# Kernel optimization log

Hardware: AMD Instinct MI355X
Metric: run time of the kernel (lower is better)

## Reference

```python
import jax, jax.numpy as jnp
import numpy as np

RADIUS = 5
WIN = (RADIUS - 1) * 2 + 1  # 9


def setup_inputs() -> dict:
    key = jax.random.key(0)
    k1, k2 = jax.random.split(key)
    B, K, H, W = 4, 4, 224, 224
    seg = jax.random.uniform(k1, (B, K, H, W), dtype=jnp.float32)
    weight = jax.random.uniform(k2, (B, 1, H, W, WIN, WIN), dtype=jnp.float32)
    return {"seg": seg, "weight": weight}


def reference(seg, weight):
    # seg: [B,K,H,W]; weight: [B,1,H,W,w,w] local affinity window, w = 2*(radius-1)+1
    B, K, H, W = seg.shape
    Kconst = jnp.float32(K)
    # torch pads by `radius` on all sides but only uses window offsets 0..2*(radius-1),
    # i.e. relative offsets [-radius, radius-2] -- replicate exactly.
    padded = jnp.pad(seg, ((0, 0), (0, 0), (RADIUS, RADIUS), (RADIUS, RADIUS)))
    # weighted sum over the local window without materializing [B,K,H,W,w,w]
    sum_w_seg = jnp.zeros_like(seg)
    for m in range(WIN):
        for n in range(WIN):
            sum_w_seg = sum_w_seg + padded[:, :, m:m + H, n:n + W] * weight[:, :, :, :, m, n]
    assocA = jnp.sum(sum_w_seg * seg, axis=(-1, -2))                      # [B,K]
    assocV = jnp.sum(jnp.sum(weight, axis=(-1, -2)) * seg, axis=(-1, -2))  # [B,K]
    assoc = jnp.sum(assocA / assocV, axis=-1)                              # [B]
    return jnp.sum(Kconst - assoc)
```

## Files before the change

### kernel.cpp

```cpp
#include <hip/hip_runtime.h>

#define RADIUS 5
#define WIN 9
#define BB 4
#define KK 4
#define HH 224
#define WW 224
#define HW (HH * WW)
#define PD 234
#define PAREA (PD * PD)
#define NBUCKET 64
#define PARTIAL_FLOATS (NBUCKET * BB * 8)
#define WAVES_PER_B (HW / 64)
#define ELEMS_PER_WAVE (64 * 81)


__global__ __launch_bounds__(256) void ncuts_pad(
    const float* __restrict__ seg, float4* __restrict__ pseg)
{
    const int tid = blockIdx.x * 256 + threadIdx.x;
    if (tid >= BB * PAREA) return;
    const int b  = tid / PAREA;
    const int rc = tid - b * PAREA;
    const int r  = rc / PD;
    const int c  = rc - r * PD;
    const int hh = r - RADIUS;
    const int ww = c - RADIUS;
    float4 v = {0.f, 0.f, 0.f, 0.f};
    if (hh >= 0 && hh < HH && ww >= 0 && ww < WW) {
        const float* sb = seg + (size_t)b * KK * HW + hh * WW + ww;
        v.x = sb[0 * HW];
        v.y = sb[1 * HW];
        v.z = sb[2 * HW];
        v.w = sb[3 * HW];
    }
    pseg[tid] = v;
}

__global__ __launch_bounds__(256, 4) void ncuts_main(
    const float* __restrict__ weight,
    const float4* __restrict__ pseg,
    float* __restrict__ partial)
{
    const int lane = threadIdx.x & 63;
    const int wid  = blockIdx.x * 4 + (threadIdx.x >> 6);
    const int b    = wid / WAVES_PER_B;

    const float* wbase = weight + (size_t)wid * ELEMS_PER_WAVE;
    const float4* p4   = pseg + (size_t)b * PAREA;

    const int pix0 = wid * 64;
    const int rem0 = pix0 - b * HW;
    int h = rem0 / WW;
    int w = rem0 - h * WW;
    int rowoff = h * PD + w;
    int tap = lane;

    float a0 = 0.f, a1 = 0.f, a2 = 0.f, a3 = 0.f;
    float v0 = 0.f, v1 = 0.f, v2 = 0.f, v3 = 0.f;

    #pragma unroll 3
    for (int t = 0; t < 81; ++t) {
        const float wv = wbase[t * 64 + lane];

        const int m = (tap * 57) >> 9;
        const int n = tap - 9 * m;

        const float4 s = p4[rowoff + m * PD + n];
        const float4 o = p4[rowoff + (RADIUS * PD + RADIUS)];

        a0 = fmaf(wv * s.x, o.x, a0);
        a1 = fmaf(wv * s.y, o.y, a1);
        a2 = fmaf(wv * s.z, o.z, a2);
        a3 = fmaf(wv * s.w, o.w, a3);
        v0 = fmaf(wv, o.x, v0);
        v1 = fmaf(wv, o.y, v1);
        v2 = fmaf(wv, o.z, v2);
        v3 = fmaf(wv, o.w, v3);

        const int t2 = tap + 64;
        const bool wrap = (t2 >= 81);
        tap = wrap ? t2 - 81 : t2;
        if (wrap) {
            const bool roww = (w == WW - 1);
            w = roww ? 0 : w + 1;
            rowoff += roww ? (PD - WW + 1) : 1;
        }
    }

    float vals[8] = { a0, a1, a2, a3, v0, v1, v2, v3 };

    #pragma unroll
    for (int i = 0; i < 8; ++i) {
        float v = vals[i];
        v += __shfl_down(v, 32);
        v += __shfl_down(v, 16);
        v += __shfl_down(v, 8);
        v += __shfl_down(v, 4);
        v += __shfl_down(v, 2);
        v += __shfl_down(v, 1);
        vals[i] = v;
    }

    if (lane == 0) {
        const int bucket = wid & (NBUCKET - 1);
        float* dst = partial + (bucket * BB + b) * 8;
        #pragma unroll
        for (int i = 0; i < 8; ++i)
            atomicAdd(dst + i, vals[i]);
    }
}

__global__ __launch_bounds__(64) void ncuts_final(
    const float* __restrict__ partial, float* __restrict__ out)
{
    __shared__ float sums[32];
    const int t = threadIdx.x;
    if (t < 32) {
        const int b = t >> 3;
        const int i = t & 7;
        float s = 0.f;
        for (int bucket = 0; bucket < NBUCKET; ++bucket)
            s += partial[(bucket * BB + b) * 8 + i];
        sums[b * 8 + i] = s;
    }
    __syncthreads();
    if (t == 0) {
        float total = 0.f;
        for (int b = 0; b < BB; ++b) {
            float assoc = 0.f;
            for (int k = 0; k < KK; ++k) {
                const float A = sums[b * 8 + k];
                const float V = sums[b * 8 + 4 + k];
                assoc += A / V;
            }
            total += (float)KK - assoc;
        }
        out[0] = total;
    }
}

extern "C" void kernel_launch(void* const* d_in, const int* in_sizes, int n_in,
                              void* d_out, int out_size, void* d_ws, size_t ws_size,
                              hipStream_t stream) {
    const float* seg    = (const float*)d_in[0];
    const float* weight = (const float*)d_in[1];
    float* out     = (float*)d_out;
    float* wsf     = (float*)d_ws;
    float* partial = wsf;
    float4* pseg   = (float4*)(wsf + PARTIAL_FLOATS);

    hipMemsetAsync(d_ws, 0, PARTIAL_FLOATS * sizeof(float), stream);

    {
        const int total = BB * PAREA;
        const int grid  = (total + 255) / 256;
        hipLaunchKernelGGL(ncuts_pad, dim3(grid), dim3(256), 0, stream, seg, pseg);
    }
    {
        const int grid = (BB * WAVES_PER_B) / 4;
        hipLaunchKernelGGL(ncuts_main, dim3(grid), dim3(256), 0, stream,
                           weight, pseg, partial);
    }
    hipLaunchKernelGGL(ncuts_final, dim3(1), dim3(64), 0, stream, partial, out);
}
```

Measured before the change: 125.0 us.

## Load weight as float4 per lane and re-map waves to smaller chunks

The main kernel now reads the weight tensor with 16-byte float4 loads, and each lane processes four consecutive window taps per iteration instead of one. Work is re-partitioned so each wave handles a 2304-element chunk over 9 iterations, which raises the wave count, and the occupancy hint in the launch bounds is dropped. Pixel and tap indices are recomputed per iteration with integer divisions, and the center value is reloaded when a tap wraps to the next pixel. This trades wider, fewer weight loads for extra index arithmetic, more divergent branches, and more scattered padded-seg gathers.

New measurement: 125.2 us. No clear change (+0.2%).

```diff
diff --git a/kernel.cpp b/kernel.cpp
--- a/kernel.cpp
+++ b/kernel.cpp
@@ -11,8 +11,11 @@
 #define PAREA (PD * PD)
 #define NBUCKET 64
 #define PARTIAL_FLOATS (NBUCKET * BB * 8)
-#define WAVES_PER_B (HW / 64)
-#define ELEMS_PER_WAVE (64 * 81)
+
+#define CHUNK_ELEMS 2304
+#define ITERS 9
+#define WAVES_PER_B 1764
+#define WAVES_TOTAL (BB * WAVES_PER_B)
 
 
 __global__ __launch_bounds__(256) void ncuts_pad(
@@ -37,8 +40,8 @@
     pseg[tid] = v;
 }
 
-__global__ __launch_bounds__(256, 4) void ncuts_main(
-    const float* __restrict__ weight,
+__global__ __launch_bounds__(256) void ncuts_main(
+    const float4* __restrict__ weight4,
     const float4* __restrict__ pseg,
     float* __restrict__ partial)
 {
@@ -46,45 +49,49 @@
     const int wid  = blockIdx.x * 4 + (threadIdx.x >> 6);
     const int b    = wid / WAVES_PER_B;
 
-    const float* wbase = weight + (size_t)wid * ELEMS_PER_WAVE;
-    const float4* p4   = pseg + (size_t)b * PAREA;
-
-    const int pix0 = wid * 64;
-    const int rem0 = pix0 - b * HW;
-    int h = rem0 / WW;
-    int w = rem0 - h * WW;
-    int rowoff = h * PD + w;
-    int tap = lane;
+    const float4* wb = weight4 + (size_t)wid * (CHUNK_ELEMS / 4);
+    const float4* pb = pseg + (size_t)b * PAREA;
 
     float a0 = 0.f, a1 = 0.f, a2 = 0.f, a3 = 0.f;
     float v0 = 0.f, v1 = 0.f, v2 = 0.f, v3 = 0.f;
 
     #pragma unroll 3
-    for (int t = 0; t < 81; ++t) {
-        const float wv = wbase[t * 64 + lane];
+    for (int t = 0; t < ITERS; ++t) {
+        const float4 wv4 = wb[t * 64 + lane];
 
-        const int m = (tap * 57) >> 9;
-        const int n = tap - 9 * m;
+        const uint32_t e0  = (uint32_t)wid * CHUNK_ELEMS + (uint32_t)(t * 256 + lane * 4);
+        const uint32_t p   = e0 / 81u;
+        int tap            = (int)(e0 - 81u * p);
+        const uint32_t rem = p - (uint32_t)b * HW;
+        uint32_t h         = rem / (uint32_t)WW;
+        uint32_t w         = rem - h * (uint32_t)WW;
+        int roff           = (int)(h * PD + w);
 
-        const float4 s = p4[rowoff + m * PD + n];
-        const float4 o = p4[rowoff + (RADIUS * PD + RADIUS)];
+        float4 o = pb[roff + RADIUS * PD + RADIUS];
+        const float wv_[4] = { wv4.x, wv4.y, wv4.z, wv4.w };
 
-        a0 = fmaf(wv * s.x, o.x, a0);
-        a1 = fmaf(wv * s.y, o.y, a1);
-        a2 = fmaf(wv * s.z, o.z, a2);
-        a3 = fmaf(wv * s.w, o.w, a3);
-        v0 = fmaf(wv, o.x, v0);
-        v1 = fmaf(wv, o.y, v1);
-        v2 = fmaf(wv, o.z, v2);
-        v3 = fmaf(wv, o.w, v3);
-
-        const int t2 = tap + 64;
-        const bool wrap = (t2 >= 81);
-        tap = wrap ? t2 - 81 : t2;
-        if (wrap) {
-            const bool roww = (w == WW - 1);
-            w = roww ? 0 : w + 1;
-            rowoff += roww ? (PD - WW + 1) : 1;
+        #pragma unroll
+        for (int j = 0; j < 4; ++j) {
+            const int m = (tap * 57) >> 9;
+            const int n = tap - 9 * m;
+            const float4 s = pb[roff + m * PD + n];
+            const float wv = wv_[j];
+            a0 = fmaf(wv * s.x, o.x, a0);
+            a1 = fmaf(wv * s.y, o.y, a1);
+            a2 = fmaf(wv * s.z, o.z, a2);
+            a3 = fmaf(wv * s.w, o.w, a3);
+            v0 = fmaf(wv, o.x, v0);
+            v1 = fmaf(wv, o.y, v1);
+            v2 = fmaf(wv, o.z, v2);
+            v3 = fmaf(wv, o.w, v3);
+            if (j < 3) {
+                if (++tap >= 81) {
+                    tap = 0;
+                    if (++w == WW) { w = 0; ++h; }
+                    roff = (int)(h * PD + w);
+                    o = pb[roff + RADIUS * PD + RADIUS];
+                }
+            }
         }
     }
 
@@ -143,8 +150,8 @@
 extern "C" void kernel_launch(void* const* d_in, const int* in_sizes, int n_in,
                               void* d_out, int out_size, void* d_ws, size_t ws_size,
                               hipStream_t stream) {
-    const float* seg    = (const float*)d_in[0];
-    const float* weight = (const float*)d_in[1];
+    const float* seg     = (const float*)d_in[0];
+    const float4* weight = (const float4*)d_in[1];
     float* out     = (float*)d_out;
     float* wsf     = (float*)d_ws;
     float* partial = wsf;
@@ -158,7 +165,7 @@
         hipLaunchKernelGGL(ncuts_pad, dim3(grid), dim3(256), 0, stream, seg, pseg);
     }
     {
-        const int grid = (BB * WAVES_PER_B) / 4;
+        const int grid = WAVES_TOTAL / 4;
         hipLaunchKernelGGL(ncuts_main, dim3(grid), dim3(256), 0, stream,
                            weight, pseg, partial);
     }
```

## Split main kernel into 1024-element weight chunks per wave with preloaded weights

Applied to the files above, without the earlier changes.

Each wave now handles a 1024-element contiguous chunk of the weight tensor (16 iterations) instead of 64 pixels × 81 taps. This launches many more, shorter waves and preloads all 16 weight values up front for memory-level parallelism. The per-lane starting pixel and tap are derived by dividing by 81. The partial-buffer memset is folded into the pad kernel, removing one stream operation. Occupancy hint raised to 6 blocks. The cost is more waves doing atomic adds and more per-wave setup arithmetic.

Result: slower. 244.8 us (+95.9%).

```diff
diff --git a/kernel.cpp b/kernel.cpp
--- a/kernel.cpp
+++ b/kernel.cpp
@@ -11,14 +11,20 @@
 #define PAREA (PD * PD)
 #define NBUCKET 64
 #define PARTIAL_FLOATS (NBUCKET * BB * 8)
-#define WAVES_PER_B (HW / 64)
-#define ELEMS_PER_WAVE (64 * 81)
+
+#define CHUNK 1024
+#define ITERS 16
+#define WAVES_PER_B (HW * 81 / CHUNK)
+#define WAVES_TOTAL (BB * WAVES_PER_B)
+#define BLOCKS_TOTAL (WAVES_TOTAL / 4)
 
 
 __global__ __launch_bounds__(256) void ncuts_pad(
-    const float* __restrict__ seg, float4* __restrict__ pseg)
+    const float* __restrict__ seg, float4* __restrict__ pseg,
+    float* __restrict__ ctrl)
 {
     const int tid = blockIdx.x * 256 + threadIdx.x;
+    if (tid < PARTIAL_FLOATS) ctrl[tid] = 0.0f;
     if (tid >= BB * PAREA) return;
     const int b  = tid / PAREA;
     const int rc = tid - b * PAREA;
@@ -37,7 +43,7 @@
     pseg[tid] = v;
 }
 
-__global__ __launch_bounds__(256, 4) void ncuts_main(
+__global__ __launch_bounds__(256, 6) void ncuts_main(
     const float* __restrict__ weight,
     const float4* __restrict__ pseg,
     float* __restrict__ partial)
@@ -46,45 +52,48 @@
     const int wid  = blockIdx.x * 4 + (threadIdx.x >> 6);
     const int b    = wid / WAVES_PER_B;
 
-    const float* wbase = weight + (size_t)wid * ELEMS_PER_WAVE;
-    const float4* p4   = pseg + (size_t)b * PAREA;
+    const float* wb  = weight + (size_t)wid * CHUNK;
+    const float4* pb = pseg + (size_t)b * PAREA;
 
-    const int pix0 = wid * 64;
-    const int rem0 = pix0 - b * HW;
-    int h = rem0 / WW;
-    int w = rem0 - h * WW;
-    int rowoff = h * PD + w;
-    int tap = lane;
+    float wv[ITERS];
+    #pragma unroll
+    for (int t = 0; t < ITERS; ++t)
+        wv[t] = wb[t * 64 + lane];
+
+    const uint32_t e0  = (uint32_t)wid * CHUNK + (uint32_t)lane;
+    const uint32_t px  = e0 / 81u;
+    int tap            = (int)(e0 - 81u * px);
+    const uint32_t rem = px - (uint32_t)b * HW;
+    uint32_t h         = rem / (uint32_t)WW;
+    uint32_t w         = rem - h * (uint32_t)WW;
+    int roff           = (int)(h * PD + w);
 
     float a0 = 0.f, a1 = 0.f, a2 = 0.f, a3 = 0.f;
     float v0 = 0.f, v1 = 0.f, v2 = 0.f, v3 = 0.f;
 
-    #pragma unroll 3
-    for (int t = 0; t < 81; ++t) {
-        const float wv = wbase[t * 64 + lane];
-
+    #pragma unroll
+    for (int t = 0; t < ITERS; ++t) {
         const int m = (tap * 57) >> 9;
         const int n = tap - 9 * m;
+        const float4 s = pb[roff + m * PD + n];
+        const float4 o = pb[roff + (RADIUS * PD + RADIUS)];
+        const float wt = wv[t];
+        a0 = fmaf(wt * s.x, o.x, a0);
+        a1 = fmaf(wt * s.y, o.y, a1);
+        a2 = fmaf(wt * s.z, o.z, a2);
+        a3 = fmaf(wt * s.w, o.w, a3);
+        v0 = fmaf(wt, o.x, v0);
+        v1 = fmaf(wt, o.y, v1);
+        v2 = fmaf(wt, o.z, v2);
+        v3 = fmaf(wt, o.w, v3);
 
-        const float4 s = p4[rowoff + m * PD + n];
-        const float4 o = p4[rowoff + (RADIUS * PD + RADIUS)];
-
-        a0 = fmaf(wv * s.x, o.x, a0);
-        a1 = fmaf(wv * s.y, o.y, a1);
-        a2 = fmaf(wv * s.z, o.z, a2);
-        a3 = fmaf(wv * s.w, o.w, a3);
-        v0 = fmaf(wv, o.x, v0);
-        v1 = fmaf(wv, o.y, v1);
-        v2 = fmaf(wv, o.z, v2);
-        v3 = fmaf(wv, o.w, v3);
-
-        const int t2 = tap + 64;
-        const bool wrap = (t2 >= 81);
-        tap = wrap ? t2 - 81 : t2;
-        if (wrap) {
+        tap += 64;
+        if (tap >= 81) {
+            tap -= 81;
             const bool roww = (w == WW - 1);
             w = roww ? 0 : w + 1;
-            rowoff += roww ? (PD - WW + 1) : 1;
+            h += roww ? 1 : 0;
+            roff += roww ? (PD - WW + 1) : 1;
         }
     }
 
@@ -150,17 +159,13 @@
     float* partial = wsf;
     float4* pseg   = (float4*)(wsf + PARTIAL_FLOATS);
 
-    hipMemsetAsync(d_ws, 0, PARTIAL_FLOATS * sizeof(float), stream);
-
     {
         const int total = BB * PAREA;
         const int grid  = (total + 255) / 256;
-        hipLaunchKernelGGL(ncuts_pad, dim3(grid), dim3(256), 0, stream, seg, pseg);
+        hipLaunchKernelGGL(ncuts_pad, dim3(grid), dim3(256), 0, stream,
+                           seg, pseg, partial);
     }
-    {
-        const int grid = (BB * WAVES_PER_B) / 4;
-        hipLaunchKernelGGL(ncuts_main, dim3(grid), dim3(256), 0, stream,
-                           weight, pseg, partial);
-    }
+    hipLaunchKernelGGL(ncuts_main, dim3(BLOCKS_TOTAL), dim3(256), 0, stream,
+                       weight, pseg, partial);
     hipLaunchKernelGGL(ncuts_final, dim3(1), dim3(64), 0, stream, partial, out);
 }
```
